# Kernel tuning notes

Hardware: AMD Instinct MI355X
Metric: run time of the kernel (lower is better)

The kernel has to match this reference:

```python
import jax, jax.numpy as jnp
import numpy as np
import math

B, S, E, H, L, FF = 32, 512, 256, 8, 4, 1024
DH = E // H
EPS = 1e-5


def layernorm(x):
    # nn.LayerNorm(elementwise_affine=False)
    m = jnp.mean(x, axis=-1, keepdims=True)
    v = jnp.mean((x - m) ** 2, axis=-1, keepdims=True)
    return (x - m) / jnp.sqrt(v + EPS)


def make_pos_embedding(e):
    vals = [math.sin(1 / 10000 ** ((i - 1) / e)) if i % 2 == 1
            else math.cos(i / 10000 ** ((i - 1) / e)) for i in range(e)]
    return jnp.asarray(np.array(vals, dtype=np.float32))


def setup_inputs() -> dict:
    key = jax.random.key(0)
    ks = jax.random.split(key, 8)
    sc = 0.02
    x = jax.random.normal(ks[0], (B, S, E), dtype=jnp.float32)
    Wq = jax.random.normal(ks[1], (L, H, DH, DH), dtype=jnp.float32) * sc
    Wk = jax.random.normal(ks[2], (L, H, DH, DH), dtype=jnp.float32) * sc
    Wv = jax.random.normal(ks[3], (L, H, DH, DH), dtype=jnp.float32) * sc
    W1 = jax.random.normal(ks[4], (L, E, FF), dtype=jnp.float32) * sc
    b1 = jnp.zeros((L, FF), dtype=jnp.float32)
    W2 = jax.random.normal(ks[5], (L, FF, E), dtype=jnp.float32) * sc
    b2 = jnp.zeros((L, E), dtype=jnp.float32)
    pos = make_pos_embedding(E)
    return {"x": x, "pos": pos, "Wq": Wq, "Wk": Wk, "Wv": Wv,
            "W1": W1, "b1": b1, "W2": W2, "b2": b2}


def encoder_layer(x, wq, wk, wv, w1, bb1, w2, bb2):
    xn = layernorm(x)
    xh = xn.reshape(B, S, H, DH)  # split embedding into per-head chunks
    q = jnp.einsum('bshd,hde->bhse', xh, wq)
    k = jnp.einsum('bshd,hde->bhse', xh, wk)
    v = jnp.einsum('bshd,hde->bhse', xh, wv)
    scores = jnp.einsum('bhsd,bhtd->bhst', q, k) / jnp.sqrt(jnp.float32(DH))
    a = jax.nn.softmax(scores, axis=-1)
    o = jnp.einsum('bhst,bhtd->bhsd', a, v)
    mha = o.transpose(0, 2, 1, 3).reshape(B, S, E)  # concat heads
    res = mha + x
    rn = layernorm(res)
    ffn = jax.nn.gelu(rn @ w1 + bb1, approximate=False) @ w2 + bb2
    return ffn + res


def reference(x, pos, Wq, Wk, Wv, W1, b1, W2, b2):
    h = x + pos  # fixed sinusoidal positional embedding
    for l in range(L):
        h = encoder_layer(h, Wq[l], Wk[l], Wv[l], W1[l], b1[l], W2[l], b2[l])
    return h
```

## Files before the change

kernel.cpp:

```cpp
#include <hip/hip_runtime.h>
#include <math.h>

#define BB   32
#define SS   512
#define EE   256
#define HH   8
#define LL   4
#define FFD  1024
#define DHD  32

constexpr float LN_EPS = 1e-5f;
constexpr int   NBSE   = BB * SS * EE;

typedef float  f32x4  __attribute__((ext_vector_type(4)));
typedef __bf16 bf16;
typedef __bf16 bf16x4 __attribute__((ext_vector_type(4)));
typedef __bf16 bf16x8 __attribute__((ext_vector_type(8)));

__device__ __forceinline__ void glds16(const bf16* g, bf16* l) {
    __builtin_amdgcn_global_load_lds(
        (const __attribute__((address_space(1))) void*)g,
        (__attribute__((address_space(3))) void*)l,
        16, 0, 0);
}

__device__ __forceinline__ float gelu_f(float x) {
    float u = x * x;
    float t = 1.5957691216057308f * x * (1.0f + 0.044715f * u);
    return x / (1.0f + __expf(-t));
}

__global__ __launch_bounds__(256) void k_cvt_t(const float* __restrict__ in,
                                               bf16* __restrict__ out,
                                               int K, int N) {
    __shared__ float tile[32][33];
    in  += (size_t)blockIdx.z * K * N;
    out += (size_t)blockIdx.z * K * N;
    int n0 = blockIdx.x * 32, k0 = blockIdx.y * 32;
    int tx = threadIdx.x & 31, ty = threadIdx.x >> 5;
    #pragma unroll
    for (int i = 0; i < 32; i += 8)
        tile[ty + i][tx] = in[(size_t)(k0 + ty + i) * N + n0 + tx];
    __syncthreads();
    #pragma unroll
    for (int i = 0; i < 32; i += 8)
        out[(size_t)(n0 + ty + i) * K + k0 + tx] = (bf16)tile[tx][ty + i];
}

__global__ __launch_bounds__(256) void k_cvt_qkv(const float* __restrict__ Wq,
                                                 const float* __restrict__ Wk,
                                                 const float* __restrict__ Wv,
                                                 bf16* __restrict__ Wqt,
                                                 bf16* __restrict__ Wkt,
                                                 bf16* __restrict__ Wvt) {
    __shared__ float tile[32][33];
    int lh = blockIdx.x;
    int z  = blockIdx.y;
    const float* in = (z == 0 ? Wq : z == 1 ? Wk : Wv) + (size_t)lh * 1024;
    bf16* out       = (z == 0 ? Wqt : z == 1 ? Wkt : Wvt) + (size_t)lh * 1024;
    float scale = (z == 0) ? 0.17677669529663687f : 1.0f;
    int tx = threadIdx.x & 31, ty = threadIdx.x >> 5;
    #pragma unroll
    for (int i = 0; i < 32; i += 8)
        tile[ty + i][tx] = in[(ty + i) * 32 + tx];
    __syncthreads();
    #pragma unroll
    for (int i = 0; i < 32; i += 8)
        out[(ty + i) * 32 + tx] = (bf16)(tile[tx][ty + i] * scale);
}

template <bool ADDPOS>
__global__ __launch_bounds__(256) void k_lnqkv(const float* __restrict__ xin,
                                               const float* __restrict__ pos,
                                               float* __restrict__ hout,
                                               const bf16* __restrict__ Wqt,
                                               const bf16* __restrict__ Wkt,
                                               const bf16* __restrict__ Wvt,
                                               bf16* __restrict__ qb,
                                               bf16* __restrict__ kb,
                                               bf16* __restrict__ vb) {
    __shared__ __attribute__((aligned(16))) bf16 Xs[64 * 264];
    int b = blockIdx.x, s0 = blockIdx.y * 64;
    int tid = threadIdx.x, w = tid >> 6, lane = tid & 63;
    size_t rowoff = ((size_t)(b * SS + s0 + w * 16)) * EE + lane * 4;
    const float* hb = xin + rowoff;
    float4 pv;
    if (ADDPOS) pv = *(const float4*)(pos + lane * 4);
    float4 xr[16];
    #pragma unroll
    for (int i = 0; i < 16; i++)
        xr[i] = *(const float4*)(hb + (size_t)i * EE);
    if (ADDPOS) {
        #pragma unroll
        for (int i = 0; i < 16; i++) {
            xr[i].x += pv.x; xr[i].y += pv.y; xr[i].z += pv.z; xr[i].w += pv.w;
            *(float4*)(hout + rowoff + (size_t)i * EE) = xr[i];
        }
    }
    #pragma unroll
    for (int i = 0; i < 16; i++) {
        float4 v4 = xr[i];
        float sum = v4.x + v4.y + v4.z + v4.w;
        #pragma unroll
        for (int m = 1; m <= 32; m <<= 1) sum += __shfl_xor(sum, m, 64);
        float mean = sum * (1.0f / EE);
        float dx = v4.x - mean, dy = v4.y - mean, dz = v4.z - mean, dw = v4.w - mean;
        float ss = dx * dx + dy * dy + dz * dz + dw * dw;
        #pragma unroll
        for (int m = 1; m <= 32; m <<= 1) ss += __shfl_xor(ss, m, 64);
        float rstd = rsqrtf(ss * (1.0f / EE) + LN_EPS);
        bf16x4 o4 = { (bf16)(dx * rstd), (bf16)(dy * rstd), (bf16)(dz * rstd), (bf16)(dw * rstd) };
        *(bf16x4*)&Xs[(w * 16 + i) * 264 + lane * 4] = o4;
    }
    __syncthreads();
    int col = lane & 15, quad = lane >> 4;
    #pragma unroll
    for (int h = 0; h < HH; h++) {
        bf16x8 a = *(const bf16x8*)&Xs[(w * 16 + col) * 264 + h * 32 + quad * 8];
        size_t base = ((size_t)((b * HH + h) * SS) + s0 + w * 16) * DHD;
        #pragma unroll
        for (int nt = 0; nt < 2; nt++) {
            int e = nt * 16 + col;
            bf16x8 bq  = *(const bf16x8*)(Wqt + (h * 32 + e) * 32 + quad * 8);
            bf16x8 bk2 = *(const bf16x8*)(Wkt + (h * 32 + e) * 32 + quad * 8);
            bf16x8 bv2 = *(const bf16x8*)(Wvt + (h * 32 + e) * 32 + quad * 8);
            f32x4 z = {0.f, 0.f, 0.f, 0.f};
            f32x4 cq = __builtin_amdgcn_mfma_f32_16x16x32_bf16(a, bq, z, 0, 0, 0);
            f32x4 ck = __builtin_amdgcn_mfma_f32_16x16x32_bf16(a, bk2, z, 0, 0, 0);
            f32x4 cv = __builtin_amdgcn_mfma_f32_16x16x32_bf16(a, bv2, z, 0, 0, 0);
            #pragma unroll
            for (int r = 0; r < 4; r++) {
                qb[base + (quad * 4 + r) * DHD + e] = (bf16)cq[r];
                kb[base + (quad * 4 + r) * DHD + e] = (bf16)ck[r];
            }
            bf16x4 vv = { (bf16)cv[0], (bf16)cv[1], (bf16)cv[2], (bf16)cv[3] };
            *(bf16x4*)&vb[(((size_t)(b * HH + h)) * DHD + e) * SS + s0 + w * 16 + quad * 4] = vv;
        }
    }
}

#define ATT_LDK 40
#define ATT_LDV 264
#define ATT_LDP 36
__global__ __launch_bounds__(256) void k_attn(const bf16* __restrict__ Q,
                                              const bf16* __restrict__ K,
                                              const bf16* __restrict__ VT,
                                              bf16* __restrict__ O) {
    __shared__ __attribute__((aligned(16))) bf16 Ks[256 * ATT_LDK];
    __shared__ __attribute__((aligned(16))) bf16 Vs[32 * ATT_LDV];
    __shared__ __attribute__((aligned(16))) bf16 Ps[4][16 * ATT_LDP];
    int bh = blockIdx.x;
    int q0 = blockIdx.y * 128;
    int tid = threadIdx.x;
    int w = tid >> 6, lane = tid & 63;
    int col = lane & 15, quad = lane >> 4;
    bf16x8 aq[2];
    #pragma unroll
    for (int sub = 0; sub < 2; sub++)
        aq[sub] = *(const bf16x8*)(Q + ((size_t)(bh * SS + q0 + sub * 64 + w * 16 + col)) * DHD + quad * 8);
    float lr[2] = {0.f, 0.f};
    f32x4 oacc[2][2] = {};
    int ksr = tid >> 2, ksc = (tid & 3) * 8;
    int vd  = tid >> 5, vso = (tid & 31) * 8;
    for (int ph = 0; ph < 2; ph++) {
        int t00 = ph * 256;
        __syncthreads();
        #pragma unroll
        for (int it = 0; it < 4; it++) {
            int rl = it * 64 + ksr;
            *(bf16x8*)&Ks[rl * ATT_LDK + ksc] =
                *(const bf16x8*)(K + ((size_t)(bh * SS + t00 + rl)) * DHD + ksc);
        }
        #pragma unroll
        for (int it = 0; it < 4; it++) {
            int d = it * 8 + vd;
            *(bf16x8*)&Vs[d * ATT_LDV + vso] =
                *(const bf16x8*)(VT + (((size_t)bh * DHD + d) * SS) + t00 + vso);
        }
        __syncthreads();
        #pragma unroll
        for (int i = 0; i < 8; i++) {
            bf16x8 bk[2], bv[2];
            #pragma unroll
            for (int nt = 0; nt < 2; nt++) {
                bk[nt] = *(const bf16x8*)&Ks[(i * 32 + nt * 16 + col) * ATT_LDK + quad * 8];
                bv[nt] = *(const bf16x8*)&Vs[(nt * 16 + col) * ATT_LDV + i * 32 + quad * 8];
            }
            #pragma unroll
            for (int sub = 0; sub < 2; sub++) {
                #pragma unroll
                for (int nt = 0; nt < 2; nt++) {
                    f32x4 z = {0.f, 0.f, 0.f, 0.f};
                    f32x4 st = __builtin_amdgcn_mfma_f32_16x16x32_bf16(bk[nt], aq[sub], z, 0, 0, 0);
                    bf16x4 p4;
                    #pragma unroll
                    for (int r = 0; r < 4; r++) {
                        float p = __expf(st[r]);
                        lr[sub] += p;
                        p4[r] = (bf16)p;
                    }
                    *(bf16x4*)&Ps[w][col * ATT_LDP + nt * 16 + quad * 4] = p4;
                }
                bf16x4 apl = *(const bf16x4*)&Ps[w][col * ATT_LDP + quad * 8];
                bf16x4 aph = *(const bf16x4*)&Ps[w][col * ATT_LDP + quad * 8 + 4];
                bf16x8 ap;
                ap[0] = apl[0]; ap[1] = apl[1]; ap[2] = apl[2]; ap[3] = apl[3];
                ap[4] = aph[0]; ap[5] = aph[1]; ap[6] = aph[2]; ap[7] = aph[3];
                #pragma unroll
                for (int nt = 0; nt < 2; nt++)
                    oacc[sub][nt] = __builtin_amdgcn_mfma_f32_16x16x32_bf16(ap, bv[nt], oacc[sub][nt], 0, 0, 0);
            }
        }
    }
    int b = bh >> 3, hh = bh & 7;
    #pragma unroll
    for (int sub = 0; sub < 2; sub++) {
        float ls = lr[sub];
        ls += __shfl_xor(ls, 16, 64);
        ls += __shfl_xor(ls, 32, 64);
        #pragma unroll
        for (int r = 0; r < 4; r++) {
            float lrow = __shfl(ls, quad * 4 + r, 64);
            float inv = 1.0f / lrow;
            int row = q0 + sub * 64 + w * 16 + quad * 4 + r;
            size_t ob = ((size_t)(b * SS + row)) * EE + hh * 32;
            O[ob + col]      = (bf16)(oacc[sub][0][r] * inv);
            O[ob + 16 + col] = (bf16)(oacc[sub][1][r] * inv);
        }
    }
}

__global__ __launch_bounds__(256) void k_resln(const bf16* __restrict__ ob,
                                               const float* __restrict__ hb,
                                               bf16* __restrict__ rn) {
    int row  = blockIdx.x * 4 + (threadIdx.x >> 6);
    int lane = threadIdx.x & 63;
    float4 h4 = *(const float4*)(hb + (size_t)row * EE + lane * 4);
    bf16x4 o4 = *(const bf16x4*)(ob + (size_t)row * EE + lane * 4);
    float v0 = h4.x + (float)o4[0], v1 = h4.y + (float)o4[1];
    float v2 = h4.z + (float)o4[2], v3 = h4.w + (float)o4[3];
    float sum = v0 + v1 + v2 + v3;
    #pragma unroll
    for (int m = 1; m <= 32; m <<= 1) sum += __shfl_xor(sum, m, 64);
    float mean = sum * (1.0f / EE);
    float d0 = v0 - mean, d1 = v1 - mean, d2 = v2 - mean, d3 = v3 - mean;
    float sq = d0 * d0 + d1 * d1 + d2 * d2 + d3 * d3;
    #pragma unroll
    for (int m = 1; m <= 32; m <<= 1) sq += __shfl_xor(sq, m, 64);
    float rstd = rsqrtf(sq * (1.0f / EE) + LN_EPS);
    bf16x4 r4 = { (bf16)(d0 * rstd), (bf16)(d1 * rstd), (bf16)(d2 * rstd), (bf16)(d3 * rstd) };
    *(bf16x4*)(rn + (size_t)row * EE + lane * 4) = r4;
}

__global__ __launch_bounds__(256) void k_gemm1(const bf16* __restrict__ A,
                                               const bf16* __restrict__ Bt,
                                               const float* __restrict__ bias,
                                               bf16* __restrict__ C) {
    __shared__ __attribute__((aligned(16))) bf16 As[128 * 32];
    __shared__ __attribute__((aligned(16))) bf16 Bs[128 * 32];
    int tid = threadIdx.x, w = tid >> 6, lane = tid & 63;
    int col = lane & 15, quad = lane >> 4;
    int wrow = w >> 1, wcol = w & 1;
    int row0 = blockIdx.x * 128, col0 = blockIdx.y * 128;
    int lrow = lane >> 2, lch = (lane & 3) * 8;
    const bf16* Ag = A  + (size_t)(row0 + w * 32 + lrow) * EE + lch;
    const bf16* Bg = Bt + (size_t)(col0 + w * 32 + lrow) * EE + lch;
    bf16* Asw = &As[(w * 32) * 32];
    bf16* Bsw = &Bs[(w * 32) * 32];
    f32x4 acc[4][4] = {};
    for (int k0 = 0; k0 < EE; k0 += 32) {
        glds16(Ag + k0, Asw);
        glds16(Ag + 16 * EE + k0, Asw + 16 * 32);
        glds16(Bg + k0, Bsw);
        glds16(Bg + 16 * EE + k0, Bsw + 16 * 32);
        __syncthreads();
        bf16x8 af[4], bf_[4];
        #pragma unroll
        for (int mt = 0; mt < 4; mt++)
            af[mt] = *(const bf16x8*)&As[(wrow * 64 + mt * 16 + col) * 32 + quad * 8];
        #pragma unroll
        for (int nt = 0; nt < 4; nt++)
            bf_[nt] = *(const bf16x8*)&Bs[(wcol * 64 + nt * 16 + col) * 32 + quad * 8];
        #pragma unroll
        for (int mt = 0; mt < 4; mt++)
            #pragma unroll
            for (int nt = 0; nt < 4; nt++)
                acc[mt][nt] = __builtin_amdgcn_mfma_f32_16x16x32_bf16(bf_[nt], af[mt], acc[mt][nt], 0, 0, 0);
        __syncthreads();
    }
    #pragma unroll
    for (int mt = 0; mt < 4; mt++) {
        int row = row0 + wrow * 64 + mt * 16 + col;
        #pragma unroll
        for (int nt = 0; nt < 4; nt++) {
            int cc = col0 + wcol * 64 + nt * 16 + quad * 4;
            float4 b4 = *(const float4*)&bias[cc];
            bf16x4 ov;
            ov[0] = (bf16)gelu_f(acc[mt][nt][0] + b4.x);
            ov[1] = (bf16)gelu_f(acc[mt][nt][1] + b4.y);
            ov[2] = (bf16)gelu_f(acc[mt][nt][2] + b4.z);
            ov[3] = (bf16)gelu_f(acc[mt][nt][3] + b4.w);
            *(bf16x4*)&C[(size_t)row * FFD + cc] = ov;
        }
    }
}

__global__ __launch_bounds__(256) void k_gemm2(const bf16* __restrict__ A,
                                               const bf16* __restrict__ Bt,
                                               const float* __restrict__ bias,
                                               const bf16* __restrict__ ob,
                                               const float* __restrict__ hb,
                                               float* __restrict__ Cf) {
    __shared__ __attribute__((aligned(16))) bf16 As[128 * 32];
    __shared__ __attribute__((aligned(16))) bf16 Bs[64 * 32];
    int tid = threadIdx.x, w = tid >> 6, lane = tid & 63;
    int col = lane & 15, quad = lane >> 4;
    int row0 = blockIdx.x * 128, col0 = blockIdx.y * 64;
    int lrow = lane >> 2, lch = (lane & 3) * 8;
    const bf16* Ag = A  + (size_t)(row0 + w * 32 + lrow) * FFD + lch;
    const bf16* Bg = Bt + (size_t)(col0 + w * 16 + lrow) * FFD + lch;
    bf16* Asw = &As[(w * 32) * 32];
    bf16* Bsw = &Bs[(w * 16) * 32];
    f32x4 acc[2][4] = {};
    for (int k0 = 0; k0 < FFD; k0 += 32) {
        glds16(Ag + k0, Asw);
        glds16(Ag + 16 * FFD + k0, Asw + 16 * 32);
        glds16(Bg + k0, Bsw);
        __syncthreads();
        bf16x8 af[2], bf_[4];
        #pragma unroll
        for (int mt = 0; mt < 2; mt++)
            af[mt] = *(const bf16x8*)&As[(w * 32 + mt * 16 + col) * 32 + quad * 8];
        #pragma unroll
        for (int nt = 0; nt < 4; nt++)
            bf_[nt] = *(const bf16x8*)&Bs[(nt * 16 + col) * 32 + quad * 8];
        #pragma unroll
        for (int mt = 0; mt < 2; mt++)
            #pragma unroll
            for (int nt = 0; nt < 4; nt++)
                acc[mt][nt] = __builtin_amdgcn_mfma_f32_16x16x32_bf16(bf_[nt], af[mt], acc[mt][nt], 0, 0, 0);
        __syncthreads();
    }
    #pragma unroll
    for (int mt = 0; mt < 2; mt++) {
        int row = row0 + w * 32 + mt * 16 + col;
        #pragma unroll
        for (int nt = 0; nt < 4; nt++) {
            int cc = col0 + nt * 16 + quad * 4;
            float4 b4 = *(const float4*)&bias[cc];
            float4 h4 = *(const float4*)&hb[(size_t)row * EE + cc];
            bf16x4 o4 = *(const bf16x4*)&ob[(size_t)row * EE + cc];
            float4 out;
            out.x = acc[mt][nt][0] + b4.x + h4.x + (float)o4[0];
            out.y = acc[mt][nt][1] + b4.y + h4.y + (float)o4[1];
            out.z = acc[mt][nt][2] + b4.z + h4.z + (float)o4[2];
            out.w = acc[mt][nt][3] + b4.w + h4.w + (float)o4[3];
            *(float4*)&Cf[(size_t)row * EE + cc] = out;
        }
    }
}

extern "C" void kernel_launch(void* const* d_in, const int* in_sizes, int n_in,
                              void* d_out, int out_size, void* d_ws, size_t ws_size,
                              hipStream_t stream) {
    (void)in_sizes; (void)n_in; (void)out_size; (void)ws_size;
    const float* x   = (const float*)d_in[0];
    const float* pos = (const float*)d_in[1];
    const float* Wq  = (const float*)d_in[2];
    const float* Wk  = (const float*)d_in[3];
    const float* Wv  = (const float*)d_in[4];
    const float* W1  = (const float*)d_in[5];
    const float* b1  = (const float*)d_in[6];
    const float* W2  = (const float*)d_in[7];
    const float* b2  = (const float*)d_in[8];

    float* ws = (float*)d_ws;
    size_t N = (size_t)NBSE;
    float* h  = ws;
    bf16* ob  = (bf16*)(ws + N);
    bf16* rnb = (bf16*)(ws + N) + N;
    bf16* qb  = (bf16*)(ws + 2 * N);
    bf16* kb  = qb + N;
    bf16* vb  = kb + N;
    bf16* ffb = (bf16*)(ws + 2 * N);
    bf16* W1t = (bf16*)(ws + 4 * N);
    bf16* W2t = W1t + (size_t)LL * EE * FFD;
    bf16* Wqt = W2t + (size_t)LL * EE * FFD;
    bf16* Wkt = Wqt + (size_t)LL * HH * DHD * DHD;
    bf16* Wvt = Wkt + (size_t)LL * HH * DHD * DHD;

    k_cvt_t<<<dim3(FFD / 32, EE / 32, LL), 256, 0, stream>>>(W1, W1t, EE, FFD);
    k_cvt_t<<<dim3(EE / 32, FFD / 32, LL), 256, 0, stream>>>(W2, W2t, FFD, EE);
    k_cvt_qkv<<<dim3(LL * HH, 3), 256, 0, stream>>>(Wq, Wk, Wv, Wqt, Wkt, Wvt);
    for (int l = 0; l < LL; l++) {
        if (l == 0)
            k_lnqkv<true><<<dim3(BB, SS / 64), 256, 0, stream>>>(
                x, pos, h, Wqt, Wkt, Wvt, qb, kb, vb);
        else
            k_lnqkv<false><<<dim3(BB, SS / 64), 256, 0, stream>>>(
                h, nullptr, nullptr,
                Wqt + (size_t)l * HH * DHD * DHD, Wkt + (size_t)l * HH * DHD * DHD,
                Wvt + (size_t)l * HH * DHD * DHD, qb, kb, vb);
        k_attn<<<dim3(BB * HH, SS / 128), 256, 0, stream>>>(qb, kb, vb, ob);
        k_resln<<<BB * SS / 4, 256, 0, stream>>>(ob, h, rnb);
        k_gemm1<<<dim3(BB * SS / 128, FFD / 128), 256, 0, stream>>>(
            rnb, W1t + (size_t)l * FFD * EE, b1 + (size_t)l * FFD, ffb);
        float* outp = (l == LL - 1) ? (float*)d_out : h;
        k_gemm2<<<dim3(BB * SS / 128, EE / 64), 256, 0, stream>>>(
            ffb, W2t + (size_t)l * EE * FFD, b2 + (size_t)l * EE, ob, h, outp);
    }
}
```

Baseline: 458.9 us.

## Fuse residual LayerNorm into FFN GEMM1, swizzle LDS, widen GEMM2 K-step

Removes the separate residual+LayerNorm kernel. GEMM1 now computes the normalized 64x256 A tile straight into XOR-swizzled shared memory and streams only B tiles. GEMM2 loads a 64-wide K slice per iteration with swizzled LDS layouts to cut bank conflicts and halve the barrier count, and the attention inner loop raises wave priority around its MFMA section. The fusion saves a global write and read of the normalized activations, but each of the four column blocks recomputes LayerNorm for its rows, and the one-pass variance formula is less numerically robust.

```diff
diff --git a/kernel.cpp b/kernel.cpp
--- a/kernel.cpp
+++ b/kernel.cpp
@@ -186,6 +186,7 @@
                 bk[nt] = *(const bf16x8*)&Ks[(i * 32 + nt * 16 + col) * ATT_LDK + quad * 8];
                 bv[nt] = *(const bf16x8*)&Vs[(nt * 16 + col) * ATT_LDV + i * 32 + quad * 8];
             }
+            __builtin_amdgcn_s_setprio(1);
             #pragma unroll
             for (int sub = 0; sub < 2; sub++) {
                 #pragma unroll
@@ -210,6 +211,7 @@
                 for (int nt = 0; nt < 2; nt++)
                     oacc[sub][nt] = __builtin_amdgcn_mfma_f32_16x16x32_bf16(ap, bv[nt], oacc[sub][nt], 0, 0, 0);
             }
+            __builtin_amdgcn_s_setprio(0);
         }
     }
     int b = bh >> 3, hh = bh & 7;
@@ -230,70 +232,74 @@
     }
 }
 
-__global__ __launch_bounds__(256) void k_resln(const bf16* __restrict__ ob,
-                                               const float* __restrict__ hb,
-                                               bf16* __restrict__ rn) {
-    int row  = blockIdx.x * 4 + (threadIdx.x >> 6);
-    int lane = threadIdx.x & 63;
-    float4 h4 = *(const float4*)(hb + (size_t)row * EE + lane * 4);
-    bf16x4 o4 = *(const bf16x4*)(ob + (size_t)row * EE + lane * 4);
-    float v0 = h4.x + (float)o4[0], v1 = h4.y + (float)o4[1];
-    float v2 = h4.z + (float)o4[2], v3 = h4.w + (float)o4[3];
-    float sum = v0 + v1 + v2 + v3;
-    #pragma unroll
-    for (int m = 1; m <= 32; m <<= 1) sum += __shfl_xor(sum, m, 64);
-    float mean = sum * (1.0f / EE);
-    float d0 = v0 - mean, d1 = v1 - mean, d2 = v2 - mean, d3 = v3 - mean;
-    float sq = d0 * d0 + d1 * d1 + d2 * d2 + d3 * d3;
-    #pragma unroll
-    for (int m = 1; m <= 32; m <<= 1) sq += __shfl_xor(sq, m, 64);
-    float rstd = rsqrtf(sq * (1.0f / EE) + LN_EPS);
-    bf16x4 r4 = { (bf16)(d0 * rstd), (bf16)(d1 * rstd), (bf16)(d2 * rstd), (bf16)(d3 * rstd) };
-    *(bf16x4*)(rn + (size_t)row * EE + lane * 4) = r4;
-}
-
-__global__ __launch_bounds__(256) void k_gemm1(const bf16* __restrict__ A,
-                                               const bf16* __restrict__ Bt,
-                                               const float* __restrict__ bias,
-                                               bf16* __restrict__ C) {
-    __shared__ __attribute__((aligned(16))) bf16 As[128 * 32];
-    __shared__ __attribute__((aligned(16))) bf16 Bs[128 * 32];
+__global__ __launch_bounds__(256, 3) void k_gemm1f(const bf16* __restrict__ ob,
+                                                   const float* __restrict__ hb,
+                                                   const bf16* __restrict__ Bt,
+                                                   const float* __restrict__ bias,
+                                                   bf16* __restrict__ C) {
+    __shared__ __attribute__((aligned(16))) bf16 As[64 * 256];
+    __shared__ __attribute__((aligned(16))) bf16 Bs[256 * 32];
     int tid = threadIdx.x, w = tid >> 6, lane = tid & 63;
     int col = lane & 15, quad = lane >> 4;
-    int wrow = w >> 1, wcol = w & 1;
-    int row0 = blockIdx.x * 128, col0 = blockIdx.y * 128;
-    int lrow = lane >> 2, lch = (lane & 3) * 8;
-    const bf16* Ag = A  + (size_t)(row0 + w * 32 + lrow) * EE + lch;
-    const bf16* Bg = Bt + (size_t)(col0 + w * 32 + lrow) * EE + lch;
-    bf16* Asw = &As[(w * 32) * 32];
-    bf16* Bsw = &Bs[(w * 32) * 32];
+    int row0 = blockIdx.x * 64, col0 = blockIdx.y * 256;
+
+    #pragma unroll 4
+    for (int rr = 0; rr < 16; rr++) {
+        int r = w * 16 + rr;
+        size_t g = (size_t)(row0 + r) * EE + lane * 4;
+        float4 h4 = *(const float4*)(hb + g);
+        bf16x4 o4 = *(const bf16x4*)(ob + g);
+        float v0 = h4.x + (float)o4[0], v1 = h4.y + (float)o4[1];
+        float v2 = h4.z + (float)o4[2], v3 = h4.w + (float)o4[3];
+        float s1 = v0 + v1 + v2 + v3;
+        float s2 = v0 * v0 + v1 * v1 + v2 * v2 + v3 * v3;
+        #pragma unroll
+        for (int m = 1; m <= 32; m <<= 1) {
+            s1 += __shfl_xor(s1, m, 64);
+            s2 += __shfl_xor(s2, m, 64);
+        }
+        float mean = s1 * (1.0f / EE);
+        float rstd = rsqrtf(s2 * (1.0f / EE) - mean * mean + LN_EPS);
+        bf16x4 a4 = { (bf16)((v0 - mean) * rstd), (bf16)((v1 - mean) * rstd),
+                      (bf16)((v2 - mean) * rstd), (bf16)((v3 - mean) * rstd) };
+        *(bf16x4*)&As[r * 256 + ((lane * 4) ^ ((r & 7) << 3))] = a4;
+    }
+
+    int bc = lane >> 2;
+    int bp = lane & 3;
     f32x4 acc[4][4] = {};
     for (int k0 = 0; k0 < EE; k0 += 32) {
-        glds16(Ag + k0, Asw);
-        glds16(Ag + 16 * EE + k0, Asw + 16 * 32);
-        glds16(Bg + k0, Bsw);
-        glds16(Bg + 16 * EE + k0, Bsw + 16 * 32);
+        __syncthreads();
+        #pragma unroll
+        for (int i = 0; i < 4; i++) {
+            int c = (w * 4 + i) * 16 + bc;
+            glds16(Bt + (size_t)(col0 + c) * EE + k0 + ((bp ^ (c & 3)) * 8),
+                   &Bs[(w * 4 + i) * 16 * 32]);
+        }
         __syncthreads();
         bf16x8 af[4], bf_[4];
         #pragma unroll
-        for (int mt = 0; mt < 4; mt++)
-            af[mt] = *(const bf16x8*)&As[(wrow * 64 + mt * 16 + col) * 32 + quad * 8];
-        #pragma unroll
-        for (int nt = 0; nt < 4; nt++)
-            bf_[nt] = *(const bf16x8*)&Bs[(wcol * 64 + nt * 16 + col) * 32 + quad * 8];
+        for (int mt = 0; mt < 4; mt++) {
+            int r = mt * 16 + col;
+            af[mt] = *(const bf16x8*)&As[r * 256 + ((k0 + quad * 8) ^ ((r & 7) << 3))];
+        }
+        #pragma unroll
+        for (int nt = 0; nt < 4; nt++) {
+            int c = w * 64 + nt * 16 + col;
+            bf_[nt] = *(const bf16x8*)&Bs[c * 32 + ((quad * 8) ^ ((c & 3) << 3))];
+        }
         #pragma unroll
         for (int mt = 0; mt < 4; mt++)
             #pragma unroll
             for (int nt = 0; nt < 4; nt++)
                 acc[mt][nt] = __builtin_amdgcn_mfma_f32_16x16x32_bf16(bf_[nt], af[mt], acc[mt][nt], 0, 0, 0);
-        __syncthreads();
     }
     #pragma unroll
     for (int mt = 0; mt < 4; mt++) {
-        int row = row0 + wrow * 64 + mt * 16 + col;
+        int row = row0 + mt * 16 + col;
         #pragma unroll
         for (int nt = 0; nt < 4; nt++) {
-            int cc = col0 + wcol * 64 + nt * 16 + quad * 4;
+            int cc = col0 + w * 64 + nt * 16 + quad * 4;
             float4 b4 = *(const float4*)&bias[cc];
             bf16x4 ov;
             ov[0] = (bf16)gelu_f(acc[mt][nt][0] + b4.x);
@@ -311,35 +317,51 @@
                                                const bf16* __restrict__ ob,
                                                const float* __restrict__ hb,
                                                float* __restrict__ Cf) {
-    __shared__ __attribute__((aligned(16))) bf16 As[128 * 32];
-    __shared__ __attribute__((aligned(16))) bf16 Bs[64 * 32];
+    __shared__ __attribute__((aligned(16))) bf16 As[128 * 64];
+    __shared__ __attribute__((aligned(16))) bf16 Bs[64 * 64];
     int tid = threadIdx.x, w = tid >> 6, lane = tid & 63;
     int col = lane & 15, quad = lane >> 4;
     int row0 = blockIdx.x * 128, col0 = blockIdx.y * 64;
-    int lrow = lane >> 2, lch = (lane & 3) * 8;
-    const bf16* Ag = A  + (size_t)(row0 + w * 32 + lrow) * FFD + lch;
-    const bf16* Bg = Bt + (size_t)(col0 + w * 16 + lrow) * FFD + lch;
-    bf16* Asw = &As[(w * 32) * 32];
-    bf16* Bsw = &Bs[(w * 16) * 32];
+    int srow = lane >> 3;
+    int spos = lane & 7;
     f32x4 acc[2][4] = {};
-    for (int k0 = 0; k0 < FFD; k0 += 32) {
-        glds16(Ag + k0, Asw);
-        glds16(Ag + 16 * FFD + k0, Asw + 16 * 32);
-        glds16(Bg + k0, Bsw);
-        __syncthreads();
-        bf16x8 af[2], bf_[4];
-        #pragma unroll
-        for (int mt = 0; mt < 2; mt++)
-            af[mt] = *(const bf16x8*)&As[(w * 32 + mt * 16 + col) * 32 + quad * 8];
-        #pragma unroll
-        for (int nt = 0; nt < 4; nt++)
-            bf_[nt] = *(const bf16x8*)&Bs[(nt * 16 + col) * 32 + quad * 8];
-        #pragma unroll
-        for (int mt = 0; mt < 2; mt++)
-            #pragma unroll
-            for (int nt = 0; nt < 4; nt++)
-                acc[mt][nt] = __builtin_amdgcn_mfma_f32_16x16x32_bf16(bf_[nt], af[mt], acc[mt][nt], 0, 0, 0);
-        __syncthreads();
+    for (int k0 = 0; k0 < FFD; k0 += 64) {
+        __syncthreads();
+        #pragma unroll
+        for (int i = 0; i < 4; i++) {
+            int r = (w * 4 + i) * 8 + srow;
+            glds16(A + (size_t)(row0 + r) * FFD + k0 + ((spos ^ (r & 7)) * 8),
+                   &As[(w * 4 + i) * 8 * 64]);
+        }
+        #pragma unroll
+        for (int i = 0; i < 2; i++) {
+            int r = (w * 2 + i) * 8 + srow;
+            glds16(Bt + (size_t)(col0 + r) * FFD + k0 + ((spos ^ (r & 7)) * 8),
+                   &Bs[(w * 2 + i) * 8 * 64]);
+        }
+        __syncthreads();
+        bf16x8 af[2][2], bf_[4][2];
+        #pragma unroll
+        for (int mt = 0; mt < 2; mt++) {
+            int r = w * 32 + mt * 16 + col;
+            #pragma unroll
+            for (int kk = 0; kk < 2; kk++)
+                af[mt][kk] = *(const bf16x8*)&As[r * 64 + ((kk * 32 + quad * 8) ^ ((r & 7) << 3))];
+        }
+        #pragma unroll
+        for (int nt = 0; nt < 4; nt++) {
+            int r = nt * 16 + col;
+            #pragma unroll
+            for (int kk = 0; kk < 2; kk++)
+                bf_[nt][kk] = *(const bf16x8*)&Bs[r * 64 + ((kk * 32 + quad * 8) ^ ((r & 7) << 3))];
+        }
+        #pragma unroll
+        for (int kk = 0; kk < 2; kk++)
+            #pragma unroll
+            for (int mt = 0; mt < 2; mt++)
+                #pragma unroll
+                for (int nt = 0; nt < 4; nt++)
+                    acc[mt][nt] = __builtin_amdgcn_mfma_f32_16x16x32_bf16(bf_[nt][kk], af[mt][kk], acc[mt][nt], 0, 0, 0);
     }
     #pragma unroll
     for (int mt = 0; mt < 2; mt++) {
@@ -378,7 +400,6 @@
     size_t N = (size_t)NBSE;
     float* h  = ws;
     bf16* ob  = (bf16*)(ws + N);
-    bf16* rnb = (bf16*)(ws + N) + N;
     bf16* qb  = (bf16*)(ws + 2 * N);
     bf16* kb  = qb + N;
     bf16* vb  = kb + N;
@@ -402,9 +423,8 @@
                 Wqt + (size_t)l * HH * DHD * DHD, Wkt + (size_t)l * HH * DHD * DHD,
                 Wvt + (size_t)l * HH * DHD * DHD, qb, kb, vb);
         k_attn<<<dim3(BB * HH, SS / 128), 256, 0, stream>>>(qb, kb, vb, ob);
-        k_resln<<<BB * SS / 4, 256, 0, stream>>>(ob, h, rnb);
-        k_gemm1<<<dim3(BB * SS / 128, FFD / 128), 256, 0, stream>>>(
-            rnb, W1t + (size_t)l * FFD * EE, b1 + (size_t)l * FFD, ffb);
+        k_gemm1f<<<dim3(BB * SS / 64, FFD / 256), 256, 0, stream>>>(
+            ob, h, W1t + (size_t)l * FFD * EE, b1 + (size_t)l * FFD, ffb);
         float* outp = (l == LL - 1) ? (float*)d_out : h;
         k_gemm2<<<dim3(BB * SS / 128, EE / 64), 256, 0, stream>>>(
             ffb, W2t + (size_t)l * EE * FFD, b2 + (size_t)l * EE, ob, h, outp);
```

Result: faster. 443.1 us (-3.5%).
